# Kernel tuning notes

Measured on AMD Instinct MI355X. Metric: run time of the kernel, lower is better.

The kernel has to match this reference:

```python
import jax, jax.numpy as jnp
import numpy as np

V, D, B, S, T, MAXLEN = 32000, 256, 4, 512, 256, 512


def _gru(x, Wih, Whh, bih, bhh):
    """torch-style GRU over x:[B,L,Din] -> [B,L,D]. Weight rows ordered [r,z,n]."""
    Dh = Whh.shape[1]
    xW = x @ Wih.T + bih  # [B,L,3D] precompute input projections

    def step(h, xw):
        hW = h @ Whh.T + bhh
        xr, xz, xn = jnp.split(xw, 3, axis=-1)
        hr, hz, hn = jnp.split(hW, 3, axis=-1)
        r = jax.nn.sigmoid(xr + hr)
        z = jax.nn.sigmoid(xz + hz)
        n = jnp.tanh(xn + r * hn)
        h = (1.0 - z) * n + z * h
        return h, h

    h0 = jnp.zeros((x.shape[0], Dh), x.dtype)
    _, ys = jax.lax.scan(step, h0, jnp.swapaxes(xW, 0, 1))
    return jnp.swapaxes(ys, 0, 1)


def setup_inputs() -> dict:
    key = jax.random.key(0)
    ks = jax.random.split(key, 24)

    def n(k, shape, scale=0.02):
        return (jax.random.normal(k, shape, jnp.float32) * scale).astype(jnp.float32)

    inp = {
        "src": jax.random.randint(ks[0], (B, S), 0, V),
        "tgt": jax.random.randint(ks[1], (B, T), 0, V),
        "emb": n(ks[2], (V, D)),
        "pos": n(ks[3], (MAXLEN, D)),
        # encoder forward direction
        "ef_wih": n(ks[4], (3 * D, D)), "ef_whh": n(ks[5], (3 * D, D)),
        "ef_bih": n(ks[6], (3 * D,)), "ef_bhh": n(ks[7], (3 * D,)),
        # encoder backward direction
        "eb_wih": n(ks[8], (3 * D, D)), "eb_whh": n(ks[9], (3 * D, D)),
        "eb_bih": n(ks[10], (3 * D,)), "eb_bhh": n(ks[11], (3 * D,)),
        # decoder
        "d_wih": n(ks[12], (3 * D, D)), "d_whh": n(ks[13], (3 * D, D)),
        "d_bih": n(ks[14], (3 * D,)), "d_bhh": n(ks[15], (3 * D,)),
        "Wq": n(ks[16], (D, D)),
        "Wk": n(ks[17], (D, 2 * D)),
        "Wgen": n(ks[18], (V, 3 * D)), "bgen": n(ks[19], (V,)),
        "Wgate": n(ks[20], (1, 3 * D)), "bgate": n(ks[21], (1,)),
    }
    return inp


def reference(src, tgt, emb, pos,
              ef_wih, ef_whh, ef_bih, ef_bhh,
              eb_wih, eb_whh, eb_bih, eb_bhh,
              d_wih, d_whh, d_bih, d_bhh,
              Wq, Wk, Wgen, bgen, Wgate, bgate):
    b, s = src.shape
    t = tgt.shape[1]
    d = emb.shape[1]
    v = emb.shape[0]

    src_emb = emb[src] + pos[:s][None]          # [B,S,D]
    enc_f = _gru(src_emb, ef_wih, ef_whh, ef_bih, ef_bhh)
    enc_b = _gru(src_emb[:, ::-1], eb_wih, eb_whh, eb_bih, eb_bhh)[:, ::-1]
    enc_out = jnp.concatenate([enc_f, enc_b], axis=-1)  # [B,S,2D]

    tgt_emb = emb[tgt] + pos[:t][None]
    dec_out = _gru(tgt_emb, d_wih, d_whh, d_bih, d_bhh)  # [B,T,D]

    Q = dec_out @ Wq.T                           # [B,T,D]
    K = enc_out @ Wk.T                           # [B,S,D]
    scores = jnp.einsum('btd,bsd->bts', Q, K) / jnp.sqrt(jnp.asarray(d, jnp.float32))
    pos_probs = jax.nn.softmax(scores, axis=-1)  # [B,T,S]

    # copy distribution: scatter attention mass into vocab buckets (== one_hot bmm)
    P_copy = jnp.zeros((b, t, v), pos_probs.dtype).at[
        jnp.arange(b)[:, None, None],
        jnp.arange(t)[None, :, None],
        src[:, None, :],
    ].add(pos_probs)

    ctx_f = jnp.einsum('bts,bsd->btd', pos_probs, enc_f)
    ctx_b = jnp.einsum('bts,bsd->btd', pos_probs, enc_b)
    combined = jnp.concatenate([dec_out, ctx_f, ctx_b], axis=-1)  # [B,T,3D]

    P_gen = jax.nn.softmax(combined @ Wgen.T + bgen, axis=-1)     # [B,T,V]
    gate = jax.nn.sigmoid(combined @ Wgate.T + bgate)             # [B,T,1]
    return gate * P_gen + (1.0 - gate) * P_copy
```

## Files before the change

kernel.cpp:

```cpp
#include <hip/hip_runtime.h>
#include <hip/hip_bf16.h>
#include <math.h>

#define VV   32000
#define DIM  256
#define BB   4
#define SS   512
#define TT   256
#define D2   512
#define D3   768

typedef __attribute__((ext_vector_type(8))) short s16x8;
typedef __attribute__((ext_vector_type(4))) float f32x4;

__device__ __forceinline__ float rcp_(float x) { return __builtin_amdgcn_rcpf(x); }
__device__ __forceinline__ float sigmoidf_(float x) { return rcp_(1.0f + __expf(-x)); }
__device__ __forceinline__ float tanhf_(float x) {
    float t = __expf(-2.0f * x);
    return (1.0f - t) * rcp_(1.0f + t);
}
__device__ __forceinline__ short f2bf(float f) {
    unsigned u = __float_as_uint(f);
    u += 0x7FFFu + ((u >> 16) & 1u);
    return (short)(u >> 16);
}

#define BAR_LGKM() asm volatile("s_waitcnt lgkmcnt(0)\n\ts_barrier" ::: "memory")

__global__ __launch_bounds__(256) void k_embed(const int* __restrict__ src,
                                               const int* __restrict__ tgt,
                                               const float* __restrict__ emb,
                                               const float* __restrict__ pos,
                                               float* __restrict__ src_emb,
                                               float* __restrict__ tgt_emb) {
    int i = blockIdx.x * 256 + threadIdx.x;
    const int nS = BB * SS * DIM;
    if (i < nS) {
        int d = i & (DIM - 1);
        int s = (i >> 8) & (SS - 1);
        int b = i >> 17;
        src_emb[i] = emb[(size_t)src[b * SS + s] * DIM + d] + pos[s * DIM + d];
    } else {
        int j = i - nS;
        int d = j & (DIM - 1);
        int t = (j >> 8) & (TT - 1);
        int b = j >> 16;
        tgt_emb[j] = emb[(size_t)tgt[b * TT + t] * DIM + d] + pos[t * DIM + d];
    }
}

__global__ __launch_bounds__(256) void k_cvt(const float* __restrict__ in,
                                             short* __restrict__ outp, int n8) {
    int i = blockIdx.x * 256 + threadIdx.x;
    if (i >= n8) return;
    const float4* p = (const float4*)(in + (size_t)i * 8);
    float4 a = p[0], b = p[1];
    s16x8 v;
    v[0] = f2bf(a.x); v[1] = f2bf(a.y); v[2] = f2bf(a.z); v[3] = f2bf(a.w);
    v[4] = f2bf(b.x); v[5] = f2bf(b.y); v[6] = f2bf(b.z); v[7] = f2bf(b.w);
    *(s16x8*)(outp + (size_t)i * 8) = v;
}

struct GDesc {
    const float* A; int lda;
    const float* Bt; int ldb;
    const float* bias;
    float* C; int ldc;
    int M, N;
};

#define BMM 128
#define BNN 128
#define BKK 8

__global__ __launch_bounds__(256) void k_gemmb(GDesc d0, GDesc d1, GDesc d2) {
    GDesc d = (blockIdx.z == 0) ? d0 : ((blockIdx.z == 1) ? d1 : d2);
    int brow = blockIdx.y * BMM, bcol = blockIdx.x * BNN;
    if (brow >= d.M || bcol >= d.N) return;

    __shared__ float As[BKK][BMM + 4];
    __shared__ float Bs[BKK][BNN + 4];
    const int K = d.lda;
    int tid = threadIdx.x;
    int tx = tid & 15, ty = tid >> 4;
    float acc[8][8];
#pragma unroll
    for (int i = 0; i < 8; i++)
#pragma unroll
        for (int j = 0; j < 8; j++) acc[i][j] = 0.0f;

    int lr = tid >> 1;
    int lk = (tid & 1) * 4;
    for (int k0 = 0; k0 < K; k0 += BKK) {
        float4 a4 = *(const float4*)&d.A[(size_t)(brow + lr) * d.lda + k0 + lk];
        float4 b4 = *(const float4*)&d.Bt[(size_t)(bcol + lr) * d.ldb + k0 + lk];
        As[lk + 0][lr] = a4.x; As[lk + 1][lr] = a4.y; As[lk + 2][lr] = a4.z; As[lk + 3][lr] = a4.w;
        Bs[lk + 0][lr] = b4.x; Bs[lk + 1][lr] = b4.y; Bs[lk + 2][lr] = b4.z; Bs[lk + 3][lr] = b4.w;
        __syncthreads();
#pragma unroll
        for (int kk = 0; kk < BKK; kk++) {
            float4 a0 = *(const float4*)&As[kk][ty * 8];
            float4 a1 = *(const float4*)&As[kk][ty * 8 + 4];
            float4 b0 = *(const float4*)&Bs[kk][tx * 8];
            float4 b1 = *(const float4*)&Bs[kk][tx * 8 + 4];
            float av[8] = {a0.x, a0.y, a0.z, a0.w, a1.x, a1.y, a1.z, a1.w};
            float bv[8] = {b0.x, b0.y, b0.z, b0.w, b1.x, b1.y, b1.z, b1.w};
#pragma unroll
            for (int i = 0; i < 8; i++)
#pragma unroll
                for (int j = 0; j < 8; j++) acc[i][j] += av[i] * bv[j];
        }
        __syncthreads();
    }

    float bv0[8];
#pragma unroll
    for (int j = 0; j < 8; j++) bv0[j] = d.bias ? d.bias[bcol + tx * 8 + j] : 0.0f;

#pragma unroll
    for (int i = 0; i < 8; i++) {
        size_t row = brow + ty * 8 + i;
        float4 c0 = make_float4(acc[i][0] + bv0[0], acc[i][1] + bv0[1],
                                acc[i][2] + bv0[2], acc[i][3] + bv0[3]);
        float4 c1 = make_float4(acc[i][4] + bv0[4], acc[i][5] + bv0[5],
                                acc[i][6] + bv0[6], acc[i][7] + bv0[7]);
        *(float4*)&d.C[row * d.ldc + bcol + tx * 8] = c0;
        *(float4*)&d.C[row * d.ldc + bcol + tx * 8 + 4] = c1;
    }
}

struct PDesc {
    const float* A;
    const float* Bt;
    const float* bias;
    float* C;
    int M;
};

__global__ __launch_bounds__(512) void k_proj(PDesc p0, PDesc p1, PDesc p2) {
    PDesc p = (blockIdx.z == 0) ? p0 : ((blockIdx.z == 1) ? p1 : p2);
    int brow = blockIdx.y * 256;
    if (brow >= p.M) return;
    int bcol = blockIdx.x * 128;

    __shared__ __align__(16) short As[256 * 32];
    __shared__ __align__(16) short Bs[128 * 32];
    int tid = threadIdx.x;
    int lane = tid & 63, wv = tid >> 6;
    int wm = wv >> 1, wn = wv & 1;
    const int ll = lane & 15, lh = lane >> 4;

    f32x4 acc[4][4];
#pragma unroll
    for (int i = 0; i < 4; i++)
#pragma unroll
        for (int j = 0; j < 4; j++) acc[i][j] = (f32x4){0.f, 0.f, 0.f, 0.f};

    const int ar = tid >> 1, ak = (tid & 1) * 16;
    const int br = tid >> 2, bk = (tid & 3) * 8;

    for (int k0 = 0; k0 < DIM; k0 += 32) {
        const float* ap = &p.A[(size_t)(brow + ar) * DIM + k0 + ak];
        float4 a0 = *(const float4*)ap;
        float4 a1 = *(const float4*)(ap + 4);
        float4 a2 = *(const float4*)(ap + 8);
        float4 a3 = *(const float4*)(ap + 12);
        const float* bp = &p.Bt[(size_t)(bcol + br) * DIM + k0 + bk];
        float4 b0 = *(const float4*)bp;
        float4 b1 = *(const float4*)(bp + 4);
        s16x8 va0, va1, vb;
        va0[0] = f2bf(a0.x); va0[1] = f2bf(a0.y); va0[2] = f2bf(a0.z); va0[3] = f2bf(a0.w);
        va0[4] = f2bf(a1.x); va0[5] = f2bf(a1.y); va0[6] = f2bf(a1.z); va0[7] = f2bf(a1.w);
        va1[0] = f2bf(a2.x); va1[1] = f2bf(a2.y); va1[2] = f2bf(a2.z); va1[3] = f2bf(a2.w);
        va1[4] = f2bf(a3.x); va1[5] = f2bf(a3.y); va1[6] = f2bf(a3.z); va1[7] = f2bf(a3.w);
        vb[0] = f2bf(b0.x); vb[1] = f2bf(b0.y); vb[2] = f2bf(b0.z); vb[3] = f2bf(b0.w);
        vb[4] = f2bf(b1.x); vb[5] = f2bf(b1.y); vb[6] = f2bf(b1.z); vb[7] = f2bf(b1.w);

        __syncthreads();
        *(s16x8*)&As[ar * 32 + ak] = va0;
        *(s16x8*)&As[ar * 32 + ak + 8] = va1;
        *(s16x8*)&Bs[br * 32 + bk] = vb;
        __syncthreads();

        s16x8 af[4], bf[4];
#pragma unroll
        for (int mt = 0; mt < 4; ++mt)
            af[mt] = *(const s16x8*)&As[(wm * 64 + mt * 16 + ll) * 32 + lh * 8];
#pragma unroll
        for (int nt = 0; nt < 4; ++nt)
            bf[nt] = *(const s16x8*)&Bs[(wn * 64 + nt * 16 + ll) * 32 + lh * 8];
#pragma unroll
        for (int mt = 0; mt < 4; ++mt)
#pragma unroll
            for (int nt = 0; nt < 4; ++nt)
                acc[mt][nt] = __builtin_amdgcn_mfma_f32_16x16x32_bf16(af[mt], bf[nt], acc[mt][nt], 0, 0, 0);
    }

#pragma unroll
    for (int mt = 0; mt < 4; ++mt) {
        int row = brow + wm * 64 + mt * 16 + lh * 4;
#pragma unroll
        for (int nt = 0; nt < 4; ++nt) {
            int col = bcol + wn * 64 + nt * 16 + ll;
            float bv = p.bias[col];
#pragma unroll
            for (int q = 0; q < 4; ++q)
                p.C[(size_t)(row + q) * D3 + col] = acc[mt][nt][q] + bv;
        }
    }
}

#define HSTRIDE 576
#define HBUF    (4 * HSTRIDE)

__global__ __launch_bounds__(512, 2) void k_gru(const float* __restrict__ ef_x,
                                                const float* __restrict__ eb_x,
                                                const float* __restrict__ d_x,
                                                const float* __restrict__ ef_whh, const float* __restrict__ ef_bhh,
                                                const float* __restrict__ eb_whh, const float* __restrict__ eb_bhh,
                                                const float* __restrict__ d_whh, const float* __restrict__ d_bhh,
                                                float* __restrict__ enc_out,
                                                float* __restrict__ dec_out) {
    __shared__ __align__(16) char hb[2 * HBUF];

    int tid = threadIdx.x;
    int dir = blockIdx.x;
    const float *xw, *Whh, *bhh;
    int L;
    if (dir == 0)      { xw = ef_x; Whh = ef_whh; bhh = ef_bhh; L = SS; }
    else if (dir == 1) { xw = eb_x; Whh = eb_whh; bhh = eb_bhh; L = SS; }
    else               { xw = d_x;  Whh = d_whh;  bhh = d_bhh;  L = TT; }

    const int wv = tid >> 6;
    const int lane = tid & 63;
    const int jj = lane & 15;
    const int hi = lane >> 4;
    const int b = hi;

    if (tid < 288) {
        f32x4 z = {0.f, 0.f, 0.f, 0.f};
        *(f32x4*)(hb + tid * 16) = z;
    }

    s16x8 wf[3][2][8];
#pragma unroll
    for (int g = 0; g < 3; ++g)
#pragma unroll
        for (int t = 0; t < 2; ++t) {
            const int nrow = g * 256 + wv * 32 + t * 16 + jj;
            const float* wp = Whh + (size_t)nrow * 256 + hi * 8;
#pragma unroll
            for (int sk = 0; sk < 8; ++sk) {
                float4 w0 = *(const float4*)(wp + sk * 32);
                float4 w1 = *(const float4*)(wp + sk * 32 + 4);
                s16x8 v;
                v[0] = f2bf(w0.x); v[1] = f2bf(w0.y); v[2] = f2bf(w0.z); v[3] = f2bf(w0.w);
                v[4] = f2bf(w1.x); v[5] = f2bf(w1.y); v[6] = f2bf(w1.z); v[7] = f2bf(w1.w);
                wf[g][t][sk] = v;
            }
        }

    const int j0 = wv * 32 + jj, j1 = j0 + 16;
    const float br0 = bhh[j0], bz0 = bhh[256 + j0], bn0 = bhh[512 + j0];
    const float br1 = bhh[j1], bz1 = bhh[256 + j1], bn1 = bhh[512 + j1];

    const int arow = jj >> 2;
    const int abase = arow * HSTRIDE + hi * 16;
    const int wo0 = b * HSTRIDE + 2 * j0;
    const int wo1 = b * HSTRIDE + 2 * j1;

    const int s0 = (dir == 1) ? (L - 1) : 0;
    const int sst = (dir == 1) ? -1 : 1;
    const float* xq = xw + ((size_t)b * L + s0) * D3 + j0;
    float* op;
    int ostride;
    if (dir == 2) { op = dec_out + ((size_t)b * TT + s0) * DIM + j0; ostride = sst * DIM; }
    else          { op = enc_out + ((size_t)b * SS + s0) * D2 + (dir == 1 ? DIM : 0) + j0; ostride = sst * D2; }
    const int xstride = sst * D3;

    float c0 = xq[0], c1 = xq[256], c2 = xq[512], c3 = xq[16], c4 = xq[272], c5 = xq[528];

    float h0 = 0.f, h1 = 0.f;
    int cur = 0;
    __syncthreads();

    for (int st = 0; st < L; ++st) {
        xq += xstride;
        float n0 = xq[0], n1 = xq[256], n2 = xq[512], n3 = xq[16], n4 = xq[272], n5 = xq[528];

        const char* hcur = hb + cur * HBUF;
        f32x4 a00 = {0.f, 0.f, 0.f, 0.f}, a01 = a00, a10 = a00, a11 = a00, a20 = a00, a21 = a00;
#pragma unroll
        for (int sk = 0; sk < 8; ++sk) {
            s16x8 af = *(const s16x8*)(hcur + abase + 64 * sk);
            a00 = __builtin_amdgcn_mfma_f32_16x16x32_bf16(af, wf[0][0][sk], a00, 0, 0, 0);
            a01 = __builtin_amdgcn_mfma_f32_16x16x32_bf16(af, wf[0][1][sk], a01, 0, 0, 0);
            a10 = __builtin_amdgcn_mfma_f32_16x16x32_bf16(af, wf[1][0][sk], a10, 0, 0, 0);
            a11 = __builtin_amdgcn_mfma_f32_16x16x32_bf16(af, wf[1][1][sk], a11, 0, 0, 0);
            a20 = __builtin_amdgcn_mfma_f32_16x16x32_bf16(af, wf[2][0][sk], a20, 0, 0, 0);
            a21 = __builtin_amdgcn_mfma_f32_16x16x32_bf16(af, wf[2][1][sk], a21, 0, 0, 0);
        }

        float r0 = sigmoidf_(c0 + a00[0] + br0);
        float z0 = sigmoidf_(c1 + a10[0] + bz0);
        float nn0 = tanhf_(c2 + r0 * (a20[0] + bn0));
        h0 = (1.f - z0) * nn0 + z0 * h0;
        float r1 = sigmoidf_(c3 + a01[0] + br1);
        float z1 = sigmoidf_(c4 + a11[0] + bz1);
        float nn1 = tanhf_(c5 + r1 * (a21[0] + bn1));
        h1 = (1.f - z1) * nn1 + z1 * h1;

        char* hnxt = hb + (cur ^ 1) * HBUF;
        *(short*)(hnxt + wo0) = f2bf(h0);
        *(short*)(hnxt + wo1) = f2bf(h1);
        op[0] = h0;
        op[16] = h1;
        BAR_LGKM();

        cur ^= 1;
        c0 = n0; c1 = n1; c2 = n2; c3 = n3; c4 = n4; c5 = n5;
        op += ostride;
    }
}

__global__ __launch_bounds__(512) void k_attn(const float* __restrict__ Qb,
                                              const float* __restrict__ Kb,
                                              const float* __restrict__ enc_out,
                                              const float* __restrict__ dec_out,
                                              const float* __restrict__ Wgate,
                                              const float* __restrict__ bgate,
                                              float* __restrict__ probs,
                                              short* __restrict__ cmb,
                                              float* __restrict__ gate) {
    __shared__ float q[DIM];
    __shared__ float sc[SS];
    __shared__ float red[512];
    __shared__ float par[2][2][DIM];
    int row = blockIdx.x;
    int b = row >> 8;
    int tid = threadIdx.x;

    if (tid < DIM) q[tid] = Qb[(size_t)row * DIM + tid];
    __syncthreads();

    const float scale = 0.0625f;
    {
        const float* kr = Kb + ((size_t)b * SS + tid) * DIM;
        float acc = 0.0f;
        for (int k = 0; k < DIM; k += 4) {
            float4 k4 = *(const float4*)&kr[k];
            acc += k4.x * q[k] + k4.y * q[k + 1] + k4.z * q[k + 2] + k4.w * q[k + 3];
        }
        sc[tid] = acc * scale;
    }
    __syncthreads();

    red[tid] = sc[tid];
    __syncthreads();
    for (int o = 256; o > 0; o >>= 1) {
        if (tid < o) red[tid] = fmaxf(red[tid], red[tid + o]);
        __syncthreads();
    }
    float m = red[0];
    __syncthreads();

    float e0 = __expf(sc[tid] - m);
    sc[tid] = e0;
    red[tid] = e0;
    __syncthreads();
    for (int o = 256; o > 0; o >>= 1) {
        if (tid < o) red[tid] += red[tid + o];
        __syncthreads();
    }
    float inv = rcp_(red[0]);
    __syncthreads();

    sc[tid] *= inv;
    probs[(size_t)row * SS + tid] = sc[tid];
    __syncthreads();

    {
        int d = tid & 255, sh = tid >> 8;
        float accf = 0.0f, accb = 0.0f;
        const float* ep = enc_out + ((size_t)b * SS + sh * 256) * D2 + d;
        const float* pp = &sc[sh * 256];
        for (int s = 0; s < 256; s++) {
            float p = pp[s];
            accf += p * ep[(size_t)s * D2];
            accb += p * ep[(size_t)s * D2 + DIM];
        }
        par[sh][0][d] = accf;
        par[sh][1][d] = accb;
    }
    __syncthreads();

    if (tid < DIM) {
        float af = par[0][0][tid] + par[1][0][tid];
        float ab = par[0][1][tid] + par[1][1][tid];
        float dv = dec_out[(size_t)row * DIM + tid];
        cmb[(size_t)row * D3 + tid] = f2bf(dv);
        cmb[(size_t)row * D3 + DIM + tid] = f2bf(af);
        cmb[(size_t)row * D3 + 2 * DIM + tid] = f2bf(ab);
        red[tid] = dv * Wgate[tid] + af * Wgate[DIM + tid] + ab * Wgate[2 * DIM + tid];
    }
    __syncthreads();
    for (int o = 128; o > 0; o >>= 1) {
        if (tid < o) red[tid] += red[tid + o];
        __syncthreads();
    }
    if (tid == 0) gate[row] = sigmoidf_(red[0] + bgate[0]);
}

__global__ __launch_bounds__(512) void k_gen_bf(const short* __restrict__ A,
                                                const short* __restrict__ Bbf,
                                                const float* __restrict__ bias,
                                                float* __restrict__ C,
                                                float* __restrict__ rowsum) {
    __shared__ __align__(16) short As[256 * 32];
    __shared__ __align__(16) short Bs[128 * 32];
    int tid = threadIdx.x;
    int lane = tid & 63, wv = tid >> 6;
    int wm = wv >> 1, wn = wv & 1;
    int brow = blockIdx.y * 256, bcol = blockIdx.x * 128;
    f32x4 acc[4][4];
#pragma unroll
    for (int i = 0; i < 4; i++)
#pragma unroll
        for (int j = 0; j < 4; j++) acc[i][j] = (f32x4){0.f, 0.f, 0.f, 0.f};

    const int ca0 = tid, ca1 = tid + 512, cb = tid;
    const int ll = lane & 15, lh = lane >> 4;

    for (int k0 = 0; k0 < D3; k0 += 32) {
        s16x8 va0 = *(const s16x8*)&A[(size_t)(brow + (ca0 >> 2)) * D3 + k0 + (ca0 & 3) * 8];
        s16x8 va1 = *(const s16x8*)&A[(size_t)(brow + (ca1 >> 2)) * D3 + k0 + (ca1 & 3) * 8];
        s16x8 vb  = *(const s16x8*)&Bbf[(size_t)(bcol + (cb >> 2)) * D3 + k0 + (cb & 3) * 8];

        __syncthreads();
        *(s16x8*)&As[ca0 * 8] = va0;
        *(s16x8*)&As[ca1 * 8] = va1;
        *(s16x8*)&Bs[cb * 8] = vb;
        __syncthreads();

        s16x8 af[4], bf[4];
#pragma unroll
        for (int mt = 0; mt < 4; ++mt)
            af[mt] = *(const s16x8*)&As[(wm * 64 + mt * 16 + ll) * 32 + lh * 8];
#pragma unroll
        for (int nt = 0; nt < 4; ++nt)
            bf[nt] = *(const s16x8*)&Bs[(wn * 64 + nt * 16 + ll) * 32 + lh * 8];
#pragma unroll
        for (int mt = 0; mt < 4; ++mt)
#pragma unroll
            for (int nt = 0; nt < 4; ++nt)
                acc[mt][nt] = __builtin_amdgcn_mfma_f32_16x16x32_bf16(af[mt], bf[nt], acc[mt][nt], 0, 0, 0);
    }

#pragma unroll
    for (int nt = 0; nt < 4; ++nt) {
        float bv = bias[bcol + wn * 64 + nt * 16 + ll];
#pragma unroll
        for (int mt = 0; mt < 4; ++mt)
#pragma unroll
            for (int q = 0; q < 4; ++q) acc[mt][nt][q] += bv;
    }

#pragma unroll
    for (int mt = 0; mt < 4; ++mt) {
        int row = brow + wm * 64 + mt * 16 + lh * 4;
#pragma unroll
        for (int nt = 0; nt < 4; ++nt) {
            int col = bcol + wn * 64 + nt * 16 + ll;
#pragma unroll
            for (int q = 0; q < 4; ++q)
                C[(size_t)(row + q) * VV + col] = acc[mt][nt][q];
        }
    }

#pragma unroll
    for (int mt = 0; mt < 4; ++mt) {
#pragma unroll
        for (int q = 0; q < 4; ++q) {
            float se = __expf(acc[mt][0][q]) + __expf(acc[mt][1][q]) +
                       __expf(acc[mt][2][q]) + __expf(acc[mt][3][q]);
#pragma unroll
            for (int off = 1; off < 16; off <<= 1)
                se += __shfl_xor(se, off);
            if (ll == 0) {
                int row = brow + wm * 64 + mt * 16 + lh * 4 + q;
                atomicAdd(&rowsum[row], se);
            }
        }
    }
}

__global__ __launch_bounds__(512) void k_gen(const short* __restrict__ A,
                                             const float* __restrict__ Bw,
                                             const float* __restrict__ bias,
                                             float* __restrict__ C,
                                             float* __restrict__ rowsum) {
    __shared__ __align__(16) short As[256 * 32];
    __shared__ __align__(16) short Bs[128 * 32];
    int tid = threadIdx.x;
    int lane = tid & 63, wv = tid >> 6;
    int wm = wv >> 1, wn = wv & 1;
    int brow = blockIdx.y * 256, bcol = blockIdx.x * 128;
    f32x4 acc[4][4];
#pragma unroll
    for (int i = 0; i < 4; i++)
#pragma unroll
        for (int j = 0; j < 4; j++) acc[i][j] = (f32x4){0.f, 0.f, 0.f, 0.f};

    const int ca0 = tid, ca1 = tid + 512, cb = tid;
    const int ll = lane & 15, lh = lane >> 4;

    for (int k0 = 0; k0 < D3; k0 += 32) {
        s16x8 va0 = *(const s16x8*)&A[(size_t)(brow + (ca0 >> 2)) * D3 + k0 + (ca0 & 3) * 8];
        s16x8 va1 = *(const s16x8*)&A[(size_t)(brow + (ca1 >> 2)) * D3 + k0 + (ca1 & 3) * 8];
        const float* bp = &Bw[(size_t)(bcol + (cb >> 2)) * D3 + k0 + (cb & 3) * 8];
        float4 b0 = *(const float4*)bp;
        float4 b1 = *(const float4*)(bp + 4);
        s16x8 vb;
        vb[0] = f2bf(b0.x); vb[1] = f2bf(b0.y); vb[2] = f2bf(b0.z); vb[3] = f2bf(b0.w);
        vb[4] = f2bf(b1.x); vb[5] = f2bf(b1.y); vb[6] = f2bf(b1.z); vb[7] = f2bf(b1.w);

        __syncthreads();
        *(s16x8*)&As[ca0 * 8] = va0;
        *(s16x8*)&As[ca1 * 8] = va1;
        *(s16x8*)&Bs[cb * 8] = vb;
        __syncthreads();

        s16x8 af[4], bf[4];
#pragma unroll
        for (int mt = 0; mt < 4; ++mt)
            af[mt] = *(const s16x8*)&As[(wm * 64 + mt * 16 + ll) * 32 + lh * 8];
#pragma unroll
        for (int nt = 0; nt < 4; ++nt)
            bf[nt] = *(const s16x8*)&Bs[(wn * 64 + nt * 16 + ll) * 32 + lh * 8];
#pragma unroll
        for (int mt = 0; mt < 4; ++mt)
#pragma unroll
            for (int nt = 0; nt < 4; ++nt)
                acc[mt][nt] = __builtin_amdgcn_mfma_f32_16x16x32_bf16(af[mt], bf[nt], acc[mt][nt], 0, 0, 0);
    }

#pragma unroll
    for (int nt = 0; nt < 4; ++nt) {
        float bv = bias[bcol + wn * 64 + nt * 16 + ll];
#pragma unroll
        for (int mt = 0; mt < 4; ++mt)
#pragma unroll
            for (int q = 0; q < 4; ++q) acc[mt][nt][q] += bv;
    }

#pragma unroll
    for (int mt = 0; mt < 4; ++mt) {
        int row = brow + wm * 64 + mt * 16 + lh * 4;
#pragma unroll
        for (int nt = 0; nt < 4; ++nt) {
            int col = bcol + wn * 64 + nt * 16 + ll;
#pragma unroll
            for (int q = 0; q < 4; ++q)
                C[(size_t)(row + q) * VV + col] = acc[mt][nt][q];
        }
    }

#pragma unroll
    for (int mt = 0; mt < 4; ++mt) {
#pragma unroll
        for (int q = 0; q < 4; ++q) {
            float se = __expf(acc[mt][0][q]) + __expf(acc[mt][1][q]) +
                       __expf(acc[mt][2][q]) + __expf(acc[mt][3][q]);
#pragma unroll
            for (int off = 1; off < 16; off <<= 1)
                se += __shfl_xor(se, off);
            if (ll == 0) {
                int row = brow + wm * 64 + mt * 16 + lh * 4 + q;
                atomicAdd(&rowsum[row], se);
            }
        }
    }
}

__global__ __launch_bounds__(256) void k_finsc(const int* __restrict__ src,
                                               const float* __restrict__ probs,
                                               const float* __restrict__ gate,
                                               const float* __restrict__ rowsum,
                                               float* __restrict__ out) {
    int row = blockIdx.x;
    int b = row >> 8;
    int tid = threadIdx.x;
    float g = gate[row];
    float inv = g / rowsum[row];
    float* op = out + (size_t)row * VV;

    for (int i = tid; i < VV / 4; i += 256) {
        float4 l = *(const float4*)&op[i * 4];
        l.x = __expf(l.x) * inv;
        l.y = __expf(l.y) * inv;
        l.z = __expf(l.z) * inv;
        l.w = __expf(l.w) * inv;
        *(float4*)&op[i * 4] = l;
    }
    __syncthreads();

    float og = 1.0f - g;
#pragma unroll
    for (int h = 0; h < 2; ++h) {
        int s = tid + h * 256;
        float val = og * probs[(size_t)row * SS + s];
        atomicAdd(&op[src[b * SS + s]], val);
    }
}

extern "C" void kernel_launch(void* const* d_in, const int* in_sizes, int n_in,
                              void* d_out, int out_size, void* d_ws, size_t ws_size,
                              hipStream_t stream) {
    const int*   src    = (const int*)d_in[0];
    const int*   tgt    = (const int*)d_in[1];
    const float* emb    = (const float*)d_in[2];
    const float* pos    = (const float*)d_in[3];
    const float* ef_wih = (const float*)d_in[4];
    const float* ef_whh = (const float*)d_in[5];
    const float* ef_bih = (const float*)d_in[6];
    const float* ef_bhh = (const float*)d_in[7];
    const float* eb_wih = (const float*)d_in[8];
    const float* eb_whh = (const float*)d_in[9];
    const float* eb_bih = (const float*)d_in[10];
    const float* eb_bhh = (const float*)d_in[11];
    const float* d_wih  = (const float*)d_in[12];
    const float* d_whh  = (const float*)d_in[13];
    const float* d_bih  = (const float*)d_in[14];
    const float* d_bhh  = (const float*)d_in[15];
    const float* Wq     = (const float*)d_in[16];
    const float* Wk     = (const float*)d_in[17];
    const float* Wgen   = (const float*)d_in[18];
    const float* bgen   = (const float*)d_in[19];
    const float* Wgate  = (const float*)d_in[20];
    const float* bgate  = (const float*)d_in[21];
    float* out = (float*)d_out;
    float* ws  = (float*)d_ws;

    float* src_emb  = ws;
    float* tgt_emb  = src_emb + (size_t)BB * SS * DIM;
    float* ef_x     = tgt_emb + (size_t)BB * TT * DIM;
    float* eb_x     = ef_x + (size_t)BB * SS * D3;
    float* d_x      = eb_x + (size_t)BB * SS * D3;
    float* enc_out  = d_x + (size_t)BB * TT * D3;
    float* dec_out  = enc_out + (size_t)BB * SS * D2;
    float* Qb       = dec_out + (size_t)BB * TT * DIM;
    float* Kb       = Qb + (size_t)BB * TT * DIM;
    float* probs    = Kb + (size_t)BB * SS * DIM;
    short* cmb_bf   = (short*)(probs + (size_t)BB * TT * SS);
    float* gate     = (float*)(cmb_bf + (size_t)BB * TT * D3);
    float* rowsum   = gate + 1024;
    short* wgen_bf  = (short*)(rowsum + 1024);
    const bool use_bf = ws_size >= (size_t)((char*)(wgen_bf + (size_t)VV * D3) - (char*)d_ws);

    hipMemsetAsync(rowsum, 0, 1024 * sizeof(float), stream);

    k_embed<<<(BB * SS * DIM + BB * TT * DIM) / 256, 256, 0, stream>>>(
        src, tgt, emb, pos, src_emb, tgt_emb);

    if (use_bf)
        k_cvt<<<(VV * D3 / 8 + 255) / 256, 256, 0, stream>>>(Wgen, wgen_bf, VV * D3 / 8);

    {
        PDesc e0 = {src_emb, ef_wih, ef_bih, ef_x, BB * SS};
        PDesc e1 = {src_emb, eb_wih, eb_bih, eb_x, BB * SS};
        PDesc e2 = {tgt_emb, d_wih, d_bih, d_x, BB * TT};
        k_proj<<<dim3(D3 / 128, BB * SS / 256, 3), 512, 0, stream>>>(e0, e1, e2);
    }

    k_gru<<<3, 512, 0, stream>>>(ef_x, eb_x, d_x, ef_whh, ef_bhh, eb_whh, eb_bhh,
                                 d_whh, d_bhh, enc_out, dec_out);

    {
        GDesc q0 = {dec_out, DIM, Wq, DIM, nullptr, Qb, DIM, BB * TT, DIM};
        GDesc q1 = {enc_out, D2, Wk, D2, nullptr, Kb, DIM, BB * SS, DIM};
        k_gemmb<<<dim3(DIM / BNN, BB * SS / BMM, 2), 256, 0, stream>>>(q0, q1, q1);
    }

    k_attn<<<BB * TT, 512, 0, stream>>>(Qb, Kb, enc_out, dec_out, Wgate, bgate,
                                        probs, cmb_bf, gate);

    if (use_bf)
        k_gen_bf<<<dim3(VV / 128, (BB * TT) / 256), 512, 0, stream>>>(cmb_bf, wgen_bf, bgen, out, rowsum);
    else
        k_gen<<<dim3(VV / 128, (BB * TT) / 256), 512, 0, stream>>>(cmb_bf, Wgen, bgen, out, rowsum);

    k_finsc<<<BB * TT, 256, 0, stream>>>(src, probs, gate, rowsum, out);
}
```

Before: 1.142 ms.

## Fuse embedding into projection, widen GRU blocks, overlap Wgen conversion with GRU

The embedding gather plus positional add moves into the input-projection GEMM's A-load, so the separate embed kernel and its intermediate buffers go away. The GRU kernel now runs with 1024 threads, so each wave handles one 16-column slice instead of two, halving per-wave MFMA and gate work on the serial recurrence. Extra blocks launched with the GRU perform the Wgen bf16 conversion and zero rowsum, overlapping that bandwidth work with the latency-bound recurrence and removing a memset and a kernel launch. The 1024-thread block raises barrier cost per step, and the conversion blocks compete for memory bandwidth with the GRU.

```diff
diff --git a/kernel.cpp b/kernel.cpp
--- a/kernel.cpp
+++ b/kernel.cpp
@@ -27,38 +27,98 @@
 
 #define BAR_LGKM() asm volatile("s_waitcnt lgkmcnt(0)\n\ts_barrier" ::: "memory")
 
-__global__ __launch_bounds__(256) void k_embed(const int* __restrict__ src,
-                                               const int* __restrict__ tgt,
-                                               const float* __restrict__ emb,
-                                               const float* __restrict__ pos,
-                                               float* __restrict__ src_emb,
-                                               float* __restrict__ tgt_emb) {
-    int i = blockIdx.x * 256 + threadIdx.x;
-    const int nS = BB * SS * DIM;
-    if (i < nS) {
-        int d = i & (DIM - 1);
-        int s = (i >> 8) & (SS - 1);
-        int b = i >> 17;
-        src_emb[i] = emb[(size_t)src[b * SS + s] * DIM + d] + pos[s * DIM + d];
-    } else {
-        int j = i - nS;
-        int d = j & (DIM - 1);
-        int t = (j >> 8) & (TT - 1);
-        int b = j >> 16;
-        tgt_emb[j] = emb[(size_t)tgt[b * TT + t] * DIM + d] + pos[t * DIM + d];
-    }
-}
-
-__global__ __launch_bounds__(256) void k_cvt(const float* __restrict__ in,
-                                             short* __restrict__ outp, int n8) {
-    int i = blockIdx.x * 256 + threadIdx.x;
-    if (i >= n8) return;
-    const float4* p = (const float4*)(in + (size_t)i * 8);
-    float4 a = p[0], b = p[1];
-    s16x8 v;
-    v[0] = f2bf(a.x); v[1] = f2bf(a.y); v[2] = f2bf(a.z); v[3] = f2bf(a.w);
-    v[4] = f2bf(b.x); v[5] = f2bf(b.y); v[6] = f2bf(b.z); v[7] = f2bf(b.w);
-    *(s16x8*)(outp + (size_t)i * 8) = v;
+struct PDesc {
+    const int* tok;
+    const float* Wt;
+    const float* bias;
+    float* C;
+    int M;
+    int lmask;
+};
+
+__global__ __launch_bounds__(512) void k_proj(const float* __restrict__ emb,
+                                              const float* __restrict__ pos,
+                                              PDesc p0, PDesc p1, PDesc p2) {
+    PDesc p = (blockIdx.z == 0) ? p0 : ((blockIdx.z == 1) ? p1 : p2);
+    int brow = blockIdx.y * 256;
+    if (brow >= p.M) return;
+    int bcol = blockIdx.x * 128;
+
+    __shared__ __align__(16) short As[256 * 32];
+    __shared__ __align__(16) short Bs[128 * 32];
+    int tid = threadIdx.x;
+    int lane = tid & 63, wv = tid >> 6;
+    int wm = wv >> 1, wn = wv & 1;
+    const int ll = lane & 15, lh = lane >> 4;
+
+    f32x4 acc[4][4];
+#pragma unroll
+    for (int i = 0; i < 4; i++)
+#pragma unroll
+        for (int j = 0; j < 4; j++) acc[i][j] = (f32x4){0.f, 0.f, 0.f, 0.f};
+
+    const int ar = tid >> 1, ak = (tid & 1) * 16;
+    const int br = tid >> 2, bk = (tid & 3) * 8;
+    const int grow = brow + ar;
+    const float* erow = emb + (size_t)p.tok[grow] * DIM;
+    const float* prow = pos + (size_t)(grow & p.lmask) * DIM;
+
+    for (int k0 = 0; k0 < DIM; k0 += 32) {
+        float4 a0 = *(const float4*)(erow + k0 + ak);
+        float4 a1 = *(const float4*)(erow + k0 + ak + 4);
+        float4 a2 = *(const float4*)(erow + k0 + ak + 8);
+        float4 a3 = *(const float4*)(erow + k0 + ak + 12);
+        float4 q0 = *(const float4*)(prow + k0 + ak);
+        float4 q1 = *(const float4*)(prow + k0 + ak + 4);
+        float4 q2 = *(const float4*)(prow + k0 + ak + 8);
+        float4 q3 = *(const float4*)(prow + k0 + ak + 12);
+        const float* bp = &p.Wt[(size_t)(bcol + br) * DIM + k0 + bk];
+        float4 b0 = *(const float4*)bp;
+        float4 b1 = *(const float4*)(bp + 4);
+        s16x8 va0, va1, vb;
+        va0[0] = f2bf(a0.x + q0.x); va0[1] = f2bf(a0.y + q0.y);
+        va0[2] = f2bf(a0.z + q0.z); va0[3] = f2bf(a0.w + q0.w);
+        va0[4] = f2bf(a1.x + q1.x); va0[5] = f2bf(a1.y + q1.y);
+        va0[6] = f2bf(a1.z + q1.z); va0[7] = f2bf(a1.w + q1.w);
+        va1[0] = f2bf(a2.x + q2.x); va1[1] = f2bf(a2.y + q2.y);
+        va1[2] = f2bf(a2.z + q2.z); va1[3] = f2bf(a2.w + q2.w);
+        va1[4] = f2bf(a3.x + q3.x); va1[5] = f2bf(a3.y + q3.y);
+        va1[6] = f2bf(a3.z + q3.z); va1[7] = f2bf(a3.w + q3.w);
+        vb[0] = f2bf(b0.x); vb[1] = f2bf(b0.y); vb[2] = f2bf(b0.z); vb[3] = f2bf(b0.w);
+        vb[4] = f2bf(b1.x); vb[5] = f2bf(b1.y); vb[6] = f2bf(b1.z); vb[7] = f2bf(b1.w);
+
+        __syncthreads();
+        *(s16x8*)&As[ar * 32 + ak] = va0;
+        *(s16x8*)&As[ar * 32 + ak + 8] = va1;
+        *(s16x8*)&Bs[br * 32 + bk] = vb;
+        __syncthreads();
+
+        s16x8 af[4], bf[4];
+#pragma unroll
+        for (int mt = 0; mt < 4; ++mt)
+            af[mt] = *(const s16x8*)&As[(wm * 64 + mt * 16 + ll) * 32 + lh * 8];
+#pragma unroll
+        for (int nt = 0; nt < 4; ++nt)
+            bf[nt] = *(const s16x8*)&Bs[(wn * 64 + nt * 16 + ll) * 32 + lh * 8];
+#pragma unroll
+        for (int mt = 0; mt < 4; ++mt)
+#pragma unroll
+            for (int nt = 0; nt < 4; ++nt)
+                acc[mt][nt] = __builtin_amdgcn_mfma_f32_16x16x32_bf16(af[mt], bf[nt], acc[mt][nt], 0, 0, 0);
+    }
+
+#pragma unroll
+    for (int mt = 0; mt < 4; ++mt) {
+        int row = brow + wm * 64 + mt * 16 + lh * 4;
+#pragma unroll
+        for (int nt = 0; nt < 4; ++nt) {
+            int col = bcol + wn * 64 + nt * 16 + ll;
+            float bv = p.bias[col];
+#pragma unroll
+            for (int q = 0; q < 4; ++q)
+                p.C[(size_t)(row + q) * D3 + col] = acc[mt][nt][q] + bv;
+        }
+    }
 }
 
 struct GDesc {
@@ -113,118 +173,54 @@
         __syncthreads();
     }
 
-    float bv0[8];
-#pragma unroll
-    for (int j = 0; j < 8; j++) bv0[j] = d.bias ? d.bias[bcol + tx * 8 + j] : 0.0f;
-
 #pragma unroll
     for (int i = 0; i < 8; i++) {
         size_t row = brow + ty * 8 + i;
-        float4 c0 = make_float4(acc[i][0] + bv0[0], acc[i][1] + bv0[1],
-                                acc[i][2] + bv0[2], acc[i][3] + bv0[3]);
-        float4 c1 = make_float4(acc[i][4] + bv0[4], acc[i][5] + bv0[5],
-                                acc[i][6] + bv0[6], acc[i][7] + bv0[7]);
+        float4 c0 = make_float4(acc[i][0], acc[i][1], acc[i][2], acc[i][3]);
+        float4 c1 = make_float4(acc[i][4], acc[i][5], acc[i][6], acc[i][7]);
         *(float4*)&d.C[row * d.ldc + bcol + tx * 8] = c0;
         *(float4*)&d.C[row * d.ldc + bcol + tx * 8 + 4] = c1;
     }
 }
 
-struct PDesc {
-    const float* A;
-    const float* Bt;
-    const float* bias;
-    float* C;
-    int M;
-};
-
-__global__ __launch_bounds__(512) void k_proj(PDesc p0, PDesc p1, PDesc p2) {
-    PDesc p = (blockIdx.z == 0) ? p0 : ((blockIdx.z == 1) ? p1 : p2);
-    int brow = blockIdx.y * 256;
-    if (brow >= p.M) return;
-    int bcol = blockIdx.x * 128;
-
-    __shared__ __align__(16) short As[256 * 32];
-    __shared__ __align__(16) short Bs[128 * 32];
-    int tid = threadIdx.x;
-    int lane = tid & 63, wv = tid >> 6;
-    int wm = wv >> 1, wn = wv & 1;
-    const int ll = lane & 15, lh = lane >> 4;
-
-    f32x4 acc[4][4];
-#pragma unroll
-    for (int i = 0; i < 4; i++)
-#pragma unroll
-        for (int j = 0; j < 4; j++) acc[i][j] = (f32x4){0.f, 0.f, 0.f, 0.f};
-
-    const int ar = tid >> 1, ak = (tid & 1) * 16;
-    const int br = tid >> 2, bk = (tid & 3) * 8;
-
-    for (int k0 = 0; k0 < DIM; k0 += 32) {
-        const float* ap = &p.A[(size_t)(brow + ar) * DIM + k0 + ak];
-        float4 a0 = *(const float4*)ap;
-        float4 a1 = *(const float4*)(ap + 4);
-        float4 a2 = *(const float4*)(ap + 8);
-        float4 a3 = *(const float4*)(ap + 12);
-        const float* bp = &p.Bt[(size_t)(bcol + br) * DIM + k0 + bk];
-        float4 b0 = *(const float4*)bp;
-        float4 b1 = *(const float4*)(bp + 4);
-        s16x8 va0, va1, vb;
-        va0[0] = f2bf(a0.x); va0[1] = f2bf(a0.y); va0[2] = f2bf(a0.z); va0[3] = f2bf(a0.w);
-        va0[4] = f2bf(a1.x); va0[5] = f2bf(a1.y); va0[6] = f2bf(a1.z); va0[7] = f2bf(a1.w);
-        va1[0] = f2bf(a2.x); va1[1] = f2bf(a2.y); va1[2] = f2bf(a2.z); va1[3] = f2bf(a2.w);
-        va1[4] = f2bf(a3.x); va1[5] = f2bf(a3.y); va1[6] = f2bf(a3.z); va1[7] = f2bf(a3.w);
-        vb[0] = f2bf(b0.x); vb[1] = f2bf(b0.y); vb[2] = f2bf(b0.z); vb[3] = f2bf(b0.w);
-        vb[4] = f2bf(b1.x); vb[5] = f2bf(b1.y); vb[6] = f2bf(b1.z); vb[7] = f2bf(b1.w);
-
-        __syncthreads();
-        *(s16x8*)&As[ar * 32 + ak] = va0;
-        *(s16x8*)&As[ar * 32 + ak + 8] = va1;
-        *(s16x8*)&Bs[br * 32 + bk] = vb;
-        __syncthreads();
-
-        s16x8 af[4], bf[4];
-#pragma unroll
-        for (int mt = 0; mt < 4; ++mt)
-            af[mt] = *(const s16x8*)&As[(wm * 64 + mt * 16 + ll) * 32 + lh * 8];
-#pragma unroll
-        for (int nt = 0; nt < 4; ++nt)
-            bf[nt] = *(const s16x8*)&Bs[(wn * 64 + nt * 16 + ll) * 32 + lh * 8];
-#pragma unroll
-        for (int mt = 0; mt < 4; ++mt)
-#pragma unroll
-            for (int nt = 0; nt < 4; ++nt)
-                acc[mt][nt] = __builtin_amdgcn_mfma_f32_16x16x32_bf16(af[mt], bf[nt], acc[mt][nt], 0, 0, 0);
-    }
-
-#pragma unroll
-    for (int mt = 0; mt < 4; ++mt) {
-        int row = brow + wm * 64 + mt * 16 + lh * 4;
-#pragma unroll
-        for (int nt = 0; nt < 4; ++nt) {
-            int col = bcol + wn * 64 + nt * 16 + ll;
-            float bv = p.bias[col];
-#pragma unroll
-            for (int q = 0; q < 4; ++q)
-                p.C[(size_t)(row + q) * D3 + col] = acc[mt][nt][q] + bv;
-        }
-    }
-}
-
 #define HSTRIDE 576
 #define HBUF    (4 * HSTRIDE)
-
-__global__ __launch_bounds__(512, 2) void k_gru(const float* __restrict__ ef_x,
-                                                const float* __restrict__ eb_x,
-                                                const float* __restrict__ d_x,
-                                                const float* __restrict__ ef_whh, const float* __restrict__ ef_bhh,
-                                                const float* __restrict__ eb_whh, const float* __restrict__ eb_bhh,
-                                                const float* __restrict__ d_whh, const float* __restrict__ d_bhh,
-                                                float* __restrict__ enc_out,
-                                                float* __restrict__ dec_out) {
+#define NCVT8   ((size_t)VV * D3 / 8)
+
+__global__ __launch_bounds__(1024) void k_gru(const float* __restrict__ ef_x,
+                                              const float* __restrict__ eb_x,
+                                              const float* __restrict__ d_x,
+                                              const float* __restrict__ ef_whh, const float* __restrict__ ef_bhh,
+                                              const float* __restrict__ eb_whh, const float* __restrict__ eb_bhh,
+                                              const float* __restrict__ d_whh, const float* __restrict__ d_bhh,
+                                              float* __restrict__ enc_out,
+                                              float* __restrict__ dec_out,
+                                              const float* __restrict__ wgen,
+                                              short* __restrict__ wgen_bf,
+                                              float* __restrict__ rowsum,
+                                              int do_cvt) {
+    int tid = threadIdx.x;
+    int bid = blockIdx.x;
+
+    if (bid >= 3) {
+        int cb = bid - 3;
+        if (cb == 0) rowsum[tid] = 0.0f;
+        if (do_cvt) {
+            size_t i = (size_t)cb * 1024 + tid;
+            if (i < NCVT8) {
+                const float4* p = (const float4*)(wgen + i * 8);
+                float4 a = p[0], b4 = p[1];
+                s16x8 v;
+                v[0] = f2bf(a.x); v[1] = f2bf(a.y); v[2] = f2bf(a.z); v[3] = f2bf(a.w);
+                v[4] = f2bf(b4.x); v[5] = f2bf(b4.y); v[6] = f2bf(b4.z); v[7] = f2bf(b4.w);
+                *(s16x8*)(wgen_bf + i * 8) = v;
+            }
+        }
+        return;
+    }
+
     __shared__ __align__(16) char hb[2 * HBUF];
-
-    int tid = threadIdx.x;
-    int dir = blockIdx.x;
+    int dir = bid;
     const float *xw, *Whh, *bhh;
     int L;
     if (dir == 0)      { xw = ef_x; Whh = ef_whh; bhh = ef_bhh; L = SS; }
@@ -242,32 +238,28 @@
         *(f32x4*)(hb + tid * 16) = z;
     }
 
-    s16x8 wf[3][2][8];
-#pragma unroll
-    for (int g = 0; g < 3; ++g)
-#pragma unroll
-        for (int t = 0; t < 2; ++t) {
-            const int nrow = g * 256 + wv * 32 + t * 16 + jj;
-            const float* wp = Whh + (size_t)nrow * 256 + hi * 8;
-#pragma unroll
-            for (int sk = 0; sk < 8; ++sk) {
-                float4 w0 = *(const float4*)(wp + sk * 32);
-                float4 w1 = *(const float4*)(wp + sk * 32 + 4);
-                s16x8 v;
-                v[0] = f2bf(w0.x); v[1] = f2bf(w0.y); v[2] = f2bf(w0.z); v[3] = f2bf(w0.w);
-                v[4] = f2bf(w1.x); v[5] = f2bf(w1.y); v[6] = f2bf(w1.z); v[7] = f2bf(w1.w);
-                wf[g][t][sk] = v;
-            }
-        }
-
-    const int j0 = wv * 32 + jj, j1 = j0 + 16;
+    s16x8 wf[3][8];
+#pragma unroll
+    for (int g = 0; g < 3; ++g) {
+        const int nrow = g * 256 + wv * 16 + jj;
+        const float* wp = Whh + (size_t)nrow * 256 + hi * 8;
+#pragma unroll
+        for (int sk = 0; sk < 8; ++sk) {
+            float4 w0 = *(const float4*)(wp + sk * 32);
+            float4 w1 = *(const float4*)(wp + sk * 32 + 4);
+            s16x8 v;
+            v[0] = f2bf(w0.x); v[1] = f2bf(w0.y); v[2] = f2bf(w0.z); v[3] = f2bf(w0.w);
+            v[4] = f2bf(w1.x); v[5] = f2bf(w1.y); v[6] = f2bf(w1.z); v[7] = f2bf(w1.w);
+            wf[g][sk] = v;
+        }
+    }
+
+    const int j0 = wv * 16 + jj;
     const float br0 = bhh[j0], bz0 = bhh[256 + j0], bn0 = bhh[512 + j0];
-    const float br1 = bhh[j1], bz1 = bhh[256 + j1], bn1 = bhh[512 + j1];
 
     const int arow = jj >> 2;
     const int abase = arow * HSTRIDE + hi * 16;
     const int wo0 = b * HSTRIDE + 2 * j0;
-    const int wo1 = b * HSTRIDE + 2 * j1;
 
     const int s0 = (dir == 1) ? (L - 1) : 0;
     const int sst = (dir == 1) ? -1 : 1;
@@ -278,47 +270,38 @@
     else          { op = enc_out + ((size_t)b * SS + s0) * D2 + (dir == 1 ? DIM : 0) + j0; ostride = sst * D2; }
     const int xstride = sst * D3;
 
-    float c0 = xq[0], c1 = xq[256], c2 = xq[512], c3 = xq[16], c4 = xq[272], c5 = xq[528];
-
-    float h0 = 0.f, h1 = 0.f;
+    float c0 = xq[0], c1 = xq[256], c2 = xq[512];
+
+    float h0 = 0.f;
     int cur = 0;
     __syncthreads();
 
     for (int st = 0; st < L; ++st) {
         xq += xstride;
-        float n0 = xq[0], n1 = xq[256], n2 = xq[512], n3 = xq[16], n4 = xq[272], n5 = xq[528];
+        float n0 = xq[0], n1 = xq[256], n2 = xq[512];
 
         const char* hcur = hb + cur * HBUF;
-        f32x4 a00 = {0.f, 0.f, 0.f, 0.f}, a01 = a00, a10 = a00, a11 = a00, a20 = a00, a21 = a00;
+        f32x4 a00 = {0.f, 0.f, 0.f, 0.f}, a10 = a00, a20 = a00;
 #pragma unroll
         for (int sk = 0; sk < 8; ++sk) {
             s16x8 af = *(const s16x8*)(hcur + abase + 64 * sk);
-            a00 = __builtin_amdgcn_mfma_f32_16x16x32_bf16(af, wf[0][0][sk], a00, 0, 0, 0);
-            a01 = __builtin_amdgcn_mfma_f32_16x16x32_bf16(af, wf[0][1][sk], a01, 0, 0, 0);
-            a10 = __builtin_amdgcn_mfma_f32_16x16x32_bf16(af, wf[1][0][sk], a10, 0, 0, 0);
-            a11 = __builtin_amdgcn_mfma_f32_16x16x32_bf16(af, wf[1][1][sk], a11, 0, 0, 0);
-            a20 = __builtin_amdgcn_mfma_f32_16x16x32_bf16(af, wf[2][0][sk], a20, 0, 0, 0);
-            a21 = __builtin_amdgcn_mfma_f32_16x16x32_bf16(af, wf[2][1][sk], a21, 0, 0, 0);
+            a00 = __builtin_amdgcn_mfma_f32_16x16x32_bf16(af, wf[0][sk], a00, 0, 0, 0);
+            a10 = __builtin_amdgcn_mfma_f32_16x16x32_bf16(af, wf[1][sk], a10, 0, 0, 0);
+            a20 = __builtin_amdgcn_mfma_f32_16x16x32_bf16(af, wf[2][sk], a20, 0, 0, 0);
         }
 
         float r0 = sigmoidf_(c0 + a00[0] + br0);
         float z0 = sigmoidf_(c1 + a10[0] + bz0);
         float nn0 = tanhf_(c2 + r0 * (a20[0] + bn0));
         h0 = (1.f - z0) * nn0 + z0 * h0;
-        float r1 = sigmoidf_(c3 + a01[0] + br1);
-        float z1 = sigmoidf_(c4 + a11[0] + bz1);
-        float nn1 = tanhf_(c5 + r1 * (a21[0] + bn1));
-        h1 = (1.f - z1) * nn1 + z1 * h1;
 
         char* hnxt = hb + (cur ^ 1) * HBUF;
         *(short*)(hnxt + wo0) = f2bf(h0);
-        *(short*)(hnxt + wo1) = f2bf(h1);
         op[0] = h0;
-        op[16] = h1;
         BAR_LGKM();
 
         cur ^= 1;
-        c0 = n0; c1 = n1; c2 = n2; c3 = n3; c4 = n4; c5 = n5;
+        c0 = n0; c1 = n1; c2 = n2;
         op += ostride;
     }
 }
@@ -641,9 +624,7 @@
     float* out = (float*)d_out;
     float* ws  = (float*)d_ws;
 
-    float* src_emb  = ws;
-    float* tgt_emb  = src_emb + (size_t)BB * SS * DIM;
-    float* ef_x     = tgt_emb + (size_t)BB * TT * DIM;
+    float* ef_x     = ws;
     float* eb_x     = ef_x + (size_t)BB * SS * D3;
     float* d_x      = eb_x + (size_t)BB * SS * D3;
     float* enc_out  = d_x + (size_t)BB * TT * D3;
@@ -657,23 +638,20 @@
     short* wgen_bf  = (short*)(rowsum + 1024);
     const bool use_bf = ws_size >= (size_t)((char*)(wgen_bf + (size_t)VV * D3) - (char*)d_ws);
 
-    hipMemsetAsync(rowsum, 0, 1024 * sizeof(float), stream);
-
-    k_embed<<<(BB * SS * DIM + BB * TT * DIM) / 256, 256, 0, stream>>>(
-        src, tgt, emb, pos, src_emb, tgt_emb);
-
-    if (use_bf)
-        k_cvt<<<(VV * D3 / 8 + 255) / 256, 256, 0, stream>>>(Wgen, wgen_bf, VV * D3 / 8);
-
     {
-        PDesc e0 = {src_emb, ef_wih, ef_bih, ef_x, BB * SS};
-        PDesc e1 = {src_emb, eb_wih, eb_bih, eb_x, BB * SS};
-        PDesc e2 = {tgt_emb, d_wih, d_bih, d_x, BB * TT};
-        k_proj<<<dim3(D3 / 128, BB * SS / 256, 3), 512, 0, stream>>>(e0, e1, e2);
-    }
-
-    k_gru<<<3, 512, 0, stream>>>(ef_x, eb_x, d_x, ef_whh, ef_bhh, eb_whh, eb_bhh,
-                                 d_whh, d_bhh, enc_out, dec_out);
+        PDesc e0 = {src, ef_wih, ef_bih, ef_x, BB * SS, SS - 1};
+        PDesc e1 = {src, eb_wih, eb_bih, eb_x, BB * SS, SS - 1};
+        PDesc e2 = {tgt, d_wih, d_bih, d_x, BB * TT, TT - 1};
+        k_proj<<<dim3(D3 / 128, BB * SS / 256, 3), 512, 0, stream>>>(emb, pos, e0, e1, e2);
+    }
+
+    {
+        int ncvtb = (int)((NCVT8 + 1023) / 1024);
+        k_gru<<<3 + ncvtb, 1024, 0, stream>>>(ef_x, eb_x, d_x,
+                                              ef_whh, ef_bhh, eb_whh, eb_bhh, d_whh, d_bhh,
+                                              enc_out, dec_out,
+                                              Wgen, wgen_bf, rowsum, use_bf ? 1 : 0);
+    }
 
     {
         GDesc q0 = {dec_out, DIM, Wq, DIM, nullptr, Qb, DIM, BB * TT, DIM};
```

New measurement: 1.072 ms. 6.1% less time.
